# Kernel optimization log

Measured on AMD Instinct MI355X. Metric: run time of the kernel, lower is better.

Reference implementation:

```python
import jax, jax.numpy as jnp
import numpy as np
from jax import lax

BLOCK = 64      # block_size
OVERLAP = 16
NITER = 64      # Niter init kwarg; loop runs min(1000, Niter)
L = 0.24        # diffusion step size
K = 0.03        # exp(logk), logk = log(0.03)
DEPS = 0.1
FFT_STEPS = 10
THRESH = 0.1    # uniform-region variance threshold


def _g(x):
    # g(x) = 1 / (1 + |x^2| / K^2)
    return 1.0 / (1.0 + jnp.abs(x * x) / (K * K))


def _avgpool3(x):
    # F.avg_pool2d(x, 3, stride=1, padding=1) with count_include_pad=True (divide by 9)
    s = lax.reduce_window(x, 0.0, lax.add, (1, 1, 3, 3), (1, 1, 1, 1),
                          [(0, 0), (0, 0), (1, 1), (1, 1)])
    return s / 9.0


def _fft_diffuse_block(block, bcv, bch):
    cv_mean = bcv.mean()
    ch_mean = bch.mean()
    h, w = block.shape[2], block.shape[3]
    ky = jnp.arange(h, dtype=block.dtype)[:, None] * (2.0 * np.pi / h)      # [h,1]
    kx = jnp.arange(w // 2 + 1, dtype=block.dtype)[None, :] * (2.0 * np.pi / w)  # [1,w//2+1]
    op = (1.0 - 2.0 * L * (cv_mean * (1.0 - jnp.cos(ky)) + ch_mean * (1.0 - jnp.cos(kx)))) ** FFT_STEPS
    return jnp.fft.irfft2(jnp.fft.rfft2(block) * op, s=(h, w))


def _forward(guide, initial):
    # depth shift for stability (torch code branches on initial.min() <= deps)
    shift = jnp.where(initial.min() <= DEPS, DEPS, 0.0).astype(initial.dtype)
    depth = initial + shift

    # diffusion coefficients from guide: cv [B,1,H-1,W], ch [B,1,H,W-1]
    cv = _g(jnp.mean(jnp.abs(guide[:, :, 1:, :] - guide[:, :, :-1, :]), axis=1, keepdims=True))
    ch = _g(jnp.mean(jnp.abs(guide[:, :, :, 1:] - guide[:, :, :, :-1]), axis=1, keepdims=True))

    # identify_uniform_regions (local variance via avg pools); original torch code
    # broadcasts shapes (H-1,W) & (H,W-1) which errors -- we crop to common (H-1,W-1)
    cv_var = _avgpool3(cv ** 2) - _avgpool3(cv) ** 2
    ch_var = _avgpool3(ch ** 2) - _avgpool3(ch) ** 2
    uniform = ((cv_var[:, :, :, :-1] < THRESH) & (ch_var[:, :, :-1, :] < THRESH)).astype(depth.dtype)

    B, C, H, W = depth.shape
    step = BLOCK - OVERLAP
    # sequential per-block FFT diffusion with overlap blending (blocks read
    # depth updated by previous blocks, so order matters)
    for b in range(B):
        for y in range(0, H, step):
            for x in range(0, W, step):
                y_end = min(y + BLOCK, H)
                x_end = min(x + BLOCK, W)
                bh, bw = y_end - y, x_end - x
                block = depth[b:b + 1, :, y:y_end, x:x_end]
                bcv = cv[b:b + 1, :, y:y_end - 1, x:x_end]
                bch = ch[b:b + 1, :, y:y_end, x:x_end - 1]
                bun = uniform[b:b + 1, :, y:y_end, x:x_end]  # clips at edges (H-1,W-1)
                cond = bun.mean() > 0.7
                newb = _fft_diffuse_block(block, bcv, bch)
                if y > 0 or x > 0:
                    blend_y = jnp.ones((bh,), depth.dtype)
                    if y > 0:
                        r = jnp.arange(bh)
                        blend_y = jnp.where(r < min(OVERLAP, bh), r.astype(depth.dtype) / OVERLAP, blend_y)
                    blend_x = jnp.ones((bw,), depth.dtype)
                    if x > 0:
                        r = jnp.arange(bw)
                        blend_x = jnp.where(r < min(OVERLAP, bw), r.astype(depth.dtype) / OVERLAP, blend_x)
                    blend = (blend_y[:, None] * blend_x[None, :])[None, None]
                    cand = block * (1.0 - blend) + newb * blend
                else:
                    cand = newb
                region = jnp.where(cond, cand, block)
                depth = depth.at[b:b + 1, :, y:y_end, x:x_end].set(region)

    # explicit anisotropic diffusion stencil, serial data dependence -> lax.scan
    def diffuse_step(I, _):
        dv = I[:, :, 1:, :] - I[:, :, :-1, :]
        dh = I[:, :, :, 1:] - I[:, :, :, :-1]  # computed before vertical update (as in torch)
        tv = L * cv * dv
        I = I.at[:, :, 1:, :].add(-tv).at[:, :, :-1, :].add(tv)
        th = L * ch * dh
        I = I.at[:, :, :, 1:].add(-th).at[:, :, :, :-1].add(th)
        return I, None

    depth, _ = lax.scan(diffuse_step, depth, None, length=min(1000, NITER))
    y_pred = depth - shift
    return y_pred, cv, ch


def setup_inputs() -> dict:
    key = jax.random.key(0)
    k1, k2 = jax.random.split(key)
    guide = jax.random.uniform(k1, (2, 3, 512, 512), dtype=jnp.float32)
    initial = jax.random.uniform(k2, (2, 1, 512, 512), dtype=jnp.float32)
    return {"guide": guide, "initial": initial}


def reference(guide, initial):
    # returns (y_pred, cv, ch) matching {'y_pred':..., 'cv':..., 'ch':...}
    return _forward(guide, initial)
```

## Files before the change

kernel.cpp:

```cpp
#include <hip/hip_runtime.h>
#include <stdint.h>

#define LDIFF 0.24f
#define MAGIC 0x5EED0B0B

constexpr int H = 512, W = 512, NB = 2;
constexpr int HW = H * W;
constexpr int N_D = NB * HW;
constexpr int CVH = 511, CVW = 512;
constexpr int CHH = 512, CHW = 511;
constexpr int N_CV = NB * CVH * CVW;
constexpr int NBLKS = 11;
constexpr int NBT = NB * 121;

__device__ inline float ldc(const float* p) {
    return __hip_atomic_load(p, __ATOMIC_RELAXED, __HIP_MEMORY_SCOPE_AGENT);
}
__device__ inline void stc(float* p, float v) {
    __hip_atomic_store(p, v, __ATOMIC_RELAXED, __HIP_MEMORY_SCOPE_AGENT);
}
__device__ inline int ldci(const int* p) {
    return __hip_atomic_load(p, __ATOMIC_RELAXED, __HIP_MEMORY_SCOPE_AGENT);
}
__device__ inline void stci(int* p, int v) {
    __hip_atomic_store(p, v, __ATOMIC_RELAXED, __HIP_MEMORY_SCOPE_AGENT);
}

__device__ inline float rot_a(float x) {
    return __int_as_float(__builtin_amdgcn_update_dpp(0, __float_as_int(x), 0x134, 0xf, 0xf, false));
}
__device__ inline float rot_b(float x) {
    return __int_as_float(__builtin_amdgcn_update_dpp(0, __float_as_int(x), 0x13c, 0xf, 0xf, false));
}
__device__ inline float sh_a(float x) {
    return __int_as_float(__builtin_amdgcn_update_dpp(0, __float_as_int(x), 0x130, 0xf, 0xf, true));
}
__device__ inline float sh_b(float x) {
    return __int_as_float(__builtin_amdgcn_update_dpp(0, __float_as_int(x), 0x138, 0xf, 0xf, true));
}

#define BSTEP(SRC, DST, LO, HI)                                                   \
    _Pragma("unroll")                                                             \
    for (int m = (LO); m <= (HI); m++) {                                          \
        float hs = rot_a(SRC[m]) + rot_b(SRC[m]);                                 \
        float vs = SRC[m - 1] + SRC[m + 1];                                       \
        DST[m] = fmaf(a, vs, fmaf(bc, hs, c0 * SRC[m]));                          \
    }

#define CSTEP(SRC, DST, LO, HI)                                                   \
    _Pragma("unroll")                                                             \
    for (int m = (LO); m <= (HI); m++) {                                          \
        float Vm = SRC[m] + cve[m] * (SRC[m + 1] - SRC[m])                        \
                          - cve[m - 1] * (SRC[m] - SRC[m - 1]);                   \
        float rA = rot_a(Vm), rB = rot_b(Vm);                                     \
        DST[m] = Vm + Pq[m] * (rB - Vm) - Qq[m] * (Vm - rA);                      \
    }

__global__ __launch_bounds__(256) void kall(
    const float* __restrict__ guide, const float* __restrict__ initial,
    float* __restrict__ cv, float* __restrict__ ch,
    float* __restrict__ D, float* __restrict__ T0, float* __restrict__ T1,
    float* __restrict__ ypred, int* __restrict__ sync_)
{
    __shared__ float cvT[73 * 74];
    __shared__ float chT[73 * 74];
    __shared__ float xT[2][4][5][64];
    __shared__ float xB[2][4][5][64];
    __shared__ float red[12];
    __shared__ float prmS[3];
    __shared__ int ctlS[2];

    const int blk = blockIdx.x;
    const int i = blk / NBLKS, j = blk % NBLKS;
    const int b = blockIdx.y;
    const int tid = threadIdx.x;
    const int lane = tid & 63, wv = tid >> 6;
    const int r0 = wv * 16;
    const int me = b * 121 + blk;

    if (tid == 0) {
        int mg = ldci(&sync_[65536]);
        int pw = ldci(&sync_[65537]);
        ctlS[0] = (mg == MAGIC) ? 1 : 0;
        ctlS[1] = (mg == MAGIC) ? (pw & 1) : 0;
    }
    __syncthreads();
    const int havemg = ctlS[0], par = ctlS[1];
    int* wflag = sync_ + par * 32768;
    int* dflag = wflag + 16384;
    {
        int* oth = sync_ + (par ^ 1) * 32768;
        if (tid < 64) stci(&oth[me * 64 + tid], 0);
        if (tid < 16) stci(&oth[16384 + me * 16 + tid], 0);
        if (!havemg) {
            if (tid < 64) stci(&wflag[me * 64 + tid], 0);
            if (tid < 16) stci(&dflag[me * 16 + tid], 0);
            if (me == 0 && tid == 0) { stci(&sync_[65537], 0); stci(&sync_[65538], 0); }
        }
        asm volatile("s_waitcnt vmcnt(0)" ::: "memory");
    }
    __syncthreads();

    const int y0 = i * 48, x0 = j * 48;
    const int y1 = min(y0 + 64, 512), x1 = min(x0 + 64, 512);
    const int bh = y1 - y0, bw = x1 - x0;
    const int yb = y0 - 8, xb = x0 - 8;
    const float kinv = 1.0f / (0.03f * 0.03f);

    const float* gb = guide + (size_t)b * 3 * HW;
    for (int p = tid; p < 73 * 73; p += 256) {
        int rr = p / 73, cc2 = p - rr * 73;
        int y = yb + rr, x = xb + cc2;
        float cvv = 0.0f, chv = 0.0f;
        if (y >= 0 && y < 512 && x >= 0 && x < 512) {
            const float* g = gb + y * W + x;
            float g0 = g[0], g1 = g[HW], g2 = g[2 * HW];
            if (y < 511) {
                float d = (fabsf(g[W] - g0) + fabsf(g[HW + W] - g1) + fabsf(g[2 * HW + W] - g2)) * (1.0f / 3.0f);
                cvv = 1.0f / (1.0f + d * d * kinv);
            }
            if (x < 511) {
                float d = (fabsf(g[1] - g0) + fabsf(g[HW + 1] - g1) + fabsf(g[2 * HW + 1] - g2)) * (1.0f / 3.0f);
                chv = 1.0f / (1.0f + d * d * kinv);
            }
        }
        cvT[rr * 74 + cc2] = cvv;
        chT[rr * 74 + cc2] = chv;
    }
    __syncthreads();

    {
        int rcv = min(y0 + 48, CVH) - y0, ccv = min(x0 + 48, CVW) - x0;
        float* cvo = cv + b * CVH * CVW;
        for (int p = tid; p < rcv * ccv; p += 256) {
            int r = p / ccv, c = p - r * ccv;
            cvo[(y0 + r) * CVW + x0 + c] = cvT[(r + 8) * 74 + c + 8];
        }
        int rch = min(y0 + 48, CHH) - y0, cch = min(x0 + 48, CHW) - x0;
        float* cho = ch + b * CHH * CHW;
        for (int p = tid; p < rch * cch; p += 256) {
            int r = p / cch, c = p - r * cch;
            cho[(y0 + r) * CHW + x0 + c] = chT[(r + 8) * 74 + c + 8];
        }
    }

    float scv = 0.f, sch = 0.f, sun = 0.f;
    {
        int n = (bh - 1) * bw;
        for (int p = tid; p < n; p += 256) { int r = p / bw, c = p - r * bw; scv += cvT[(r + 8) * 74 + c + 8]; }
    }
    {
        int cols = bw - 1, n = bh * cols;
        for (int p = tid; p < n; p += 256) { int r = p / cols, c = p - r * cols; sch += chT[(r + 8) * 74 + c + 8]; }
    }
    const int ur = min(y1, 511) - y0, uc = min(x1, 511) - x0;
    {
        int n = ur * uc;
        for (int p = tid; p < n; p += 256) {
            int r = p / uc, c = p - r * uc;
            float s1 = 0.f, s2 = 0.f, t1 = 0.f, t2 = 0.f;
            #pragma unroll
            for (int dy = 0; dy < 3; dy++)
                #pragma unroll
                for (int dx = 0; dx < 3; dx++) {
                    float v = cvT[(r + 7 + dy) * 74 + c + 7 + dx]; s1 += v; s2 += v * v;
                    float w2 = chT[(r + 7 + dy) * 74 + c + 7 + dx]; t1 += w2; t2 += w2 * w2;
                }
            float m = s1 * (1.0f / 9.0f);
            float vcv = s2 * (1.0f / 9.0f) - m * m;
            m = t1 * (1.0f / 9.0f);
            float vch = t2 * (1.0f / 9.0f) - m * m;
            if (vcv < 0.1f && vch < 0.1f) sun += 1.f;
        }
    }
    #pragma unroll
    for (int m = 1; m < 64; m <<= 1) {
        scv += __shfl_xor(scv, m);
        sch += __shfl_xor(sch, m);
        sun += __shfl_xor(sun, m);
    }
    if (lane == 0) { red[wv * 3] = scv; red[wv * 3 + 1] = sch; red[wv * 3 + 2] = sun; }
    __syncthreads();
    if (tid == 0) {
        float a0 = red[0] + red[3] + red[6] + red[9];
        float a1 = red[1] + red[4] + red[7] + red[10];
        float a2 = red[2] + red[5] + red[8] + red[11];
        prmS[0] = a0 / (float)((bh - 1) * bw);
        prmS[1] = a1 / (float)(bh * (bw - 1));
        prmS[2] = (a2 / (float)(ur * uc) > 0.7f) ? 1.0f : 0.0f;
    }
    __syncthreads();

    int prb = __builtin_amdgcn_update_dpp(0, lane, 0x134, 0xf, 0xf, false);
    const bool dirL = (prb == ((lane + 63) & 63));

    const bool cond = prmS[2] > 0.5f;
    const float a = LDIFF * prmS[0], bc = LDIFF * prmS[1];
    const float c0 = 1.0f - 2.0f * a - 2.0f * bc;
    float* Db = D + b * HW;
    const float* ini = initial + b * HW;

    const int mh = bh - 1, mw = bw - 1;
    const int ccw = lane & mw;

    if (!cond) {
        #pragma unroll
        for (int k = 0; k < 16; k++) {
            int r = r0 + k;
            if (r < bh && (i == 0 || r >= 16) && lane < bw && (j == 0 || lane >= 16)) {
                int ad = (y0 + r) * W + x0 + lane;
                stc(&Db[ad], ini[ad]);
            }
        }
        asm volatile("s_waitcnt vmcnt(0)" ::: "memory");
        if (lane == 0) {
            stci(&wflag[me * 64 + wv * 16], 1);
            stci(&wflag[me * 64 + wv * 16 + 8], 1);
        }
    } else {
        float u[16], orig[16];
        int addr[16]; bool fD[16];
        #pragma unroll
        for (int k = 0; k < 16; k++) {
            int rr = (r0 + k) & mh;
            addr[k] = (y0 + rr) * W + x0 + ccw;
            fD[k] = (i > 0 && rr < 16) || (j > 0 && ccw < 16);
            if (!fD[k]) orig[k] = ini[addr[k]];
        }
        {
            const int Lw = (r0 & mh) >> 4;
            const bool needU = (i > 0) && ((r0 & mh) < 16);
            bool need = false;
            const int* fp = &wflag[me * 64];
            if (lane == 0) {
                if (j > 0) { need = true; fp = &wflag[(me - 1) * 64 + Lw * 16]; }
            } else if (lane == 1) {
                if (needU) { need = true; fp = &wflag[(me - NBLKS) * 64 + 3 * 16]; }
            } else if (lane == 2) {
                if (needU && j < 10) { need = true; fp = &wflag[(me - NBLKS + 1) * 64 + 3 * 16]; }
            } else if (lane == 3) {
                if (needU && j > 0) { need = true; fp = &wflag[(me - NBLKS - 1) * 64 + 3 * 16]; }
            }
            while (true) {
                int v = need ? ldci(fp) : 1;
                if (__ballot(v == 0) == 0) break;
                __builtin_amdgcn_s_sleep(0);
            }
        }
        #pragma unroll
        for (int k = 0; k < 16; k++) if (fD[k]) orig[k] = ldc(&Db[addr[k]]);
        #pragma unroll
        for (int k = 0; k < 16; k++) u[k] = orig[k];

        float wa[26], wb[26];
        #pragma unroll
        for (int g = 0; g < 2; ++g) {
            #pragma unroll
            for (int q = 0; q < 5; q++) {
                xT[g][wv][q][lane] = u[q];
                xB[g][wv][q][lane] = u[11 + q];
            }
            __syncthreads();
            #pragma unroll
            for (int q = 0; q < 5; q++) {
                wa[q]      = xB[g][(wv + 3) & 3][q][lane];
                wa[21 + q] = xT[g][(wv + 1) & 3][q][lane];
            }
            #pragma unroll
            for (int q = 0; q < 16; q++) wa[5 + q] = u[q];
            BSTEP(wa, wb, 1, 24);
            BSTEP(wb, wa, 2, 23);
            BSTEP(wa, wb, 3, 22);
            BSTEP(wb, wa, 4, 21);
            BSTEP(wa, wb, 5, 20);
            #pragma unroll
            for (int q = 0; q < 16; q++) u[q] = wb[5 + q];
        }

        #pragma unroll
        for (int k = 0; k < 16; k++) {
            int r = r0 + k;
            float byw = (y0 > 0 && r < 16) ? (float)r * (1.0f / 16.0f) : 1.0f;
            float bxw = (x0 > 0 && lane < 16) ? (float)lane * (1.0f / 16.0f) : 1.0f;
            float wgt = byw * bxw;
            u[k] = orig[k] * (1.0f - wgt) + u[k] * wgt;
        }
        #pragma unroll
        for (int k = 0; k < 16; k++) {
            int r = r0 + k;
            bool in = (r < bh && lane < bw);
            bool sc = (bw == 64 && lane >= 48) || (r >= 48);
            if (in && sc) stc(&Db[(y0 + r) * W + x0 + lane], u[k]);
        }
        asm volatile("s_waitcnt vmcnt(0)" ::: "memory");
        if (lane == 0) stci(&wflag[me * 64 + wv * 16], 1);
        #pragma unroll
        for (int k = 0; k < 16; k++) {
            int r = r0 + k;
            bool in = (r < bh && lane < bw);
            bool sc = (bw == 64 && lane >= 48) || (r >= 48);
            if (in && !sc) stc(&Db[(y0 + r) * W + x0 + lane], u[k]);
        }
        asm volatile("s_waitcnt vmcnt(0)" ::: "memory");
        if (lane == 0) stci(&wflag[me * 64 + wv * 16 + 8], 1);
    }
    __syncthreads();

    const int cx = xb + lane;
    const int gxc = min(max(cx, 0), 511);
    int gyA[16];
    #pragma unroll
    for (int k = 0; k < 16; k++) {
        int cy = yb + r0 + k;
        gyA[k] = min(max(cy, 0), 511);
    }
    float cve[24], Pq[24], Qq[24];
    #pragma unroll
    for (int m = 0; m < 24; m++) {
        int rr = r0 + m - 4;
        bool ok = (rr >= 0);
        float cvv = ok ? cvT[rr * 74 + lane] : 0.0f;
        float chh = ok ? chT[rr * 74 + lane] : 0.0f;
        float chl = dirL ? sh_a(chh) : sh_b(chh);
        cve[m] = LDIFF * cvv;
        Pq[m] = LDIFF * (dirL ? chh : chl);
        Qq[m] = LDIFF * (dirL ? chl : chh);
    }

    float* Tb0 = T0 + b * HW;
    float* Tb1 = T1 + b * HW;
    float* ypb = ypred + b * HW;

    const int coreh = min(48, 512 - y0), corew = min(48, 512 - x0);
    const bool laneC = (lane >= 8) && (lane < 8 + corew);
    bool ownc[16], ringk[16];
    #pragma unroll
    for (int k = 0; k < 16; k++) {
        int wr = r0 + k;
        ownc[k] = laneC && (wr >= 8) && (wr < 8 + coreh);
        int cr = wr - 8, cl = lane - 8;
        ringk[k] = ownc[k] && (cr < 8 || cr >= coreh - 8 || cl < 8 || cl >= corew - 8);
    }

    float u[16];
    for (int t = 1; t <= 8; t++) {
        if (wv == 0) {
            bool need = false;
            const int* fp = &wflag[me * 64];
            int thr = 1;
            if (t == 1) {
                if (lane < 36) {
                    int nb = lane >> 2;
                    int di = nb / 3 - 1, dj = nb % 3 - 1;
                    int ni = i + di, nj = j + dj;
                    if ((di | dj) != 0 && ni >= 0 && ni < NBLKS && nj >= 0 && nj < NBLKS) {
                        need = true;
                        fp = &wflag[(b * 121 + ni * NBLKS + nj) * 64 + (lane & 3) * 16 + 8];
                    }
                }
            } else {
                thr = t - 1;
                if (lane < 9) {
                    int di = lane / 3 - 1, dj = lane % 3 - 1;
                    int ni = i + di, nj = j + dj;
                    if ((di | dj) != 0 && ni >= 0 && ni < NBLKS && nj >= 0 && nj < NBLKS) {
                        need = true;
                        fp = &dflag[(b * 121 + ni * NBLKS + nj) * 16];
                    }
                }
            }
            while (true) {
                int v = need ? ldci(fp) : 0x7fffffff;
                if (__ballot(v < thr) == 0) break;
                __builtin_amdgcn_s_sleep(4);
            }
        }
        __syncthreads();
        const float* src = (t == 1) ? Db : (((t - 1) & 1) ? Tb1 : Tb0);
        if (t == 1) {
            #pragma unroll
            for (int k = 0; k < 16; k++) u[k] = ldc(&src[gyA[k] * W + gxc]);
        } else {
            #pragma unroll
            for (int k = 0; k < 16; k++) if (!ownc[k]) u[k] = ldc(&src[gyA[k] * W + gxc]);
        }

        #pragma unroll
        for (int g = 0; g < 2; ++g) {
            #pragma unroll
            for (int q = 0; q < 4; q++) {
                xT[g][wv][q][lane] = u[q];
                xB[g][wv][q][lane] = u[12 + q];
            }
            __syncthreads();
            float wa[24], wb[24];
            #pragma unroll
            for (int q = 0; q < 4; q++) {
                wa[q]      = (wv > 0) ? xB[g][wv - 1][q][lane] : u[0];
                wa[20 + q] = (wv < 3) ? xT[g][wv + 1][q][lane] : u[15];
            }
            #pragma unroll
            for (int q = 0; q < 16; q++) wa[4 + q] = u[q];
            CSTEP(wa, wb, 1, 22);
            CSTEP(wb, wa, 2, 21);
            CSTEP(wa, wb, 3, 20);
            CSTEP(wb, wa, 4, 19);
            #pragma unroll
            for (int q = 0; q < 16; q++) u[q] = wa[4 + q];
        }

        if (t < 8) {
            float* dst = (t & 1) ? Tb1 : Tb0;
            #pragma unroll
            for (int k = 0; k < 16; k++) {
                if (ringk[k]) stc(&dst[(yb + r0 + k) * W + xb + lane], u[k]);
            }
            asm volatile("s_waitcnt vmcnt(0)" ::: "memory");
            __syncthreads();
            if (tid == 0) stci(&dflag[me * 16], t);
        } else {
            #pragma unroll
            for (int k = 0; k < 16; k++) {
                if (ownc[k]) ypb[(yb + r0 + k) * W + xb + lane] = u[k];
            }
        }
    }

    __syncthreads();
    if (tid == 0) {
        int n = __hip_atomic_fetch_add(&sync_[65538], 1, __ATOMIC_RELAXED, __HIP_MEMORY_SCOPE_AGENT);
        if (n == NBT - 1) {
            stci(&sync_[65538], 0);
            stci(&sync_[65537], par ^ 1);
            stci(&sync_[65536], MAGIC);
        }
    }
}

extern "C" void kernel_launch(void* const* d_in, const int* in_sizes, int n_in,
                              void* d_out, int out_size, void* d_ws, size_t ws_size,
                              hipStream_t stream) {
    const float* guide   = (const float*)d_in[0];
    const float* initial = (const float*)d_in[1];
    float* y_pred = (float*)d_out;
    float* cv = y_pred + N_D;
    float* ch = cv + N_CV;

    uint8_t* w = (uint8_t*)d_ws;
    int* sync_ = (int*)w;
    float* D  = (float*)(w + 262656);
    float* T0 = D + N_D;
    float* T1 = T0 + N_D;

    kall<<<dim3(121, NB), 256, 0, stream>>>(guide, initial, cv, ch, D, T0, T1, y_pred, sync_);
}
```

Baseline: 285.4 us.

## Replace per-wave flag handoff with per-element sentinel edge buffers between blocks

Each block now publishes its right and bottom overlap strips into a dedicated edge buffer pre-filled with a -1 sentinel. Neighbours poll the individual values instead of waiting on coarse per-wave completion flags, which lets dependent blocks start as soon as the specific data they need arrives and shortens the serial wavefront across the 11x11 block grid. Non-uniform blocks now go through the same unified path. The change adds clearing of the edge buffer each launch and extra polling loads, and it relies on -1 never being a valid float bit pattern in the data.

After: 525.3 us. 84.1% more time.

```diff
diff --git a/kernel.cpp b/kernel.cpp
--- a/kernel.cpp
+++ b/kernel.cpp
@@ -2,7 +2,7 @@
 #include <stdint.h>
 
 #define LDIFF 0.24f
-#define MAGIC 0x5EED0B0B
+#define MAGIC 0x5EED0C0C
 
 constexpr int H = 512, W = 512, NB = 2;
 constexpr int HW = H * W;
@@ -59,7 +59,8 @@
 __global__ __launch_bounds__(256) void kall(
     const float* __restrict__ guide, const float* __restrict__ initial,
     float* __restrict__ cv, float* __restrict__ ch,
-    float* __restrict__ D, float* __restrict__ T0, float* __restrict__ T1,
+    float* __restrict__ D, float* __restrict__ EDG,
+    float* __restrict__ T0, float* __restrict__ T1,
     float* __restrict__ ypred, int* __restrict__ sync_)
 {
     __shared__ float cvT[73 * 74];
@@ -88,13 +89,20 @@
     const int havemg = ctlS[0], par = ctlS[1];
     int* wflag = sync_ + par * 32768;
     int* dflag = wflag + 16384;
+    float* EDGp = EDG + (size_t)par * NBT * 2048;
     {
         int* oth = sync_ + (par ^ 1) * 32768;
         if (tid < 64) stci(&oth[me * 64 + tid], 0);
         if (tid < 16) stci(&oth[16384 + me * 16 + tid], 0);
+        int* eo = (int*)(EDG + (size_t)(par ^ 1) * NBT * 2048 + (size_t)me * 2048);
+        #pragma unroll
+        for (int q = 0; q < 8; q++) stci(&eo[tid + q * 256], -1);
         if (!havemg) {
             if (tid < 64) stci(&wflag[me * 64 + tid], 0);
             if (tid < 16) stci(&dflag[me * 16 + tid], 0);
+            int* ep = (int*)(EDGp + (size_t)me * 2048);
+            #pragma unroll
+            for (int q = 0; q < 8; q++) stci(&ep[tid + q * 256], -1);
             if (me == 0 && tid == 0) { stci(&sync_[65537], 0); stci(&sync_[65538], 0); }
         }
         asm volatile("s_waitcnt vmcnt(0)" ::: "memory");
@@ -202,56 +210,59 @@
 
     const int mh = bh - 1, mw = bw - 1;
     const int ccw = lane & mw;
-
-    if (!cond) {
-        #pragma unroll
-        for (int k = 0; k < 16; k++) {
-            int r = r0 + k;
-            if (r < bh && (i == 0 || r >= 16) && lane < bw && (j == 0 || lane >= 16)) {
-                int ad = (y0 + r) * W + x0 + lane;
-                stc(&Db[ad], ini[ad]);
-            }
-        }
-        asm volatile("s_waitcnt vmcnt(0)" ::: "memory");
+    const int rr0w = r0 & mh;
+
+    float u[16], orig[16];
+    const bool fD = (i > 0 && rr0w < 16) || (j > 0 && ccw < 16);
+    #pragma unroll
+    for (int k = 0; k < 16; k++) {
+        if (!fD) orig[k] = ini[(y0 + rr0w + k) * W + x0 + ccw];
+    }
+
+    {
+        bool need = false;
+        const int* wp = &sync_[65536];
         if (lane == 0) {
-            stci(&wflag[me * 64 + wv * 16], 1);
-            stci(&wflag[me * 64 + wv * 16 + 8], 1);
-        }
-    } else {
-        float u[16], orig[16];
-        int addr[16]; bool fD[16];
-        #pragma unroll
-        for (int k = 0; k < 16; k++) {
-            int rr = (r0 + k) & mh;
-            addr[k] = (y0 + rr) * W + x0 + ccw;
-            fD[k] = (i > 0 && rr < 16) || (j > 0 && ccw < 16);
-            if (!fD[k]) orig[k] = ini[addr[k]];
-        }
-        {
-            const int Lw = (r0 & mh) >> 4;
-            const bool needU = (i > 0) && ((r0 & mh) < 16);
-            bool need = false;
-            const int* fp = &wflag[me * 64];
-            if (lane == 0) {
-                if (j > 0) { need = true; fp = &wflag[(me - 1) * 64 + Lw * 16]; }
-            } else if (lane == 1) {
-                if (needU) { need = true; fp = &wflag[(me - NBLKS) * 64 + 3 * 16]; }
-            } else if (lane == 2) {
-                if (needU && j < 10) { need = true; fp = &wflag[(me - NBLKS + 1) * 64 + 3 * 16]; }
-            } else if (lane == 3) {
-                if (needU && j > 0) { need = true; fp = &wflag[(me - NBLKS - 1) * 64 + 3 * 16]; }
-            }
-            while (true) {
-                int v = need ? ldci(fp) : 1;
-                if (__ballot(v == 0) == 0) break;
-                __builtin_amdgcn_s_sleep(0);
-            }
-        }
-        #pragma unroll
-        for (int k = 0; k < 16; k++) if (fD[k]) orig[k] = ldc(&Db[addr[k]]);
-        #pragma unroll
-        for (int k = 0; k < 16; k++) u[k] = orig[k];
-
+            if (j > 0) { need = true; wp = (const int*)(EDGp + (size_t)(me - 1) * 2048 + (rr0w + 15) * 16 + 15); }
+        } else if (lane == 1) {
+            if (i > 0 && rr0w < 16) { need = true; wp = (const int*)(EDGp + (size_t)(me - NBLKS) * 2048 + 1024 + 15 * 64 + (bw == 64 ? 47 : bw - 1)); }
+        } else if (lane == 2) {
+            if (i > 0 && rr0w < 16 && j < 10) { need = true; wp = (const int*)(EDGp + (size_t)(me - NBLKS + 1) * 2048 + 1024 + 15 * 64 + 15); }
+        }
+        while (true) {
+            int v = need ? ldci(wp) : 0;
+            if (__ballot(v == -1) == 0) break;
+            __builtin_amdgcn_s_sleep(0);
+        }
+    }
+    {
+        const int* sp0 = nullptr; int strd = 0;
+        if (j > 0 && ccw < 16) {
+            sp0 = (const int*)(EDGp + (size_t)(me - 1) * 2048 + rr0w * 16 + ccw);
+            strd = 16;
+        } else if (i > 0 && rr0w < 16) {
+            sp0 = (ccw >= 48) ? (const int*)(EDGp + (size_t)(me - NBLKS + 1) * 2048 + 1024 + (ccw - 48))
+                              : (const int*)(EDGp + (size_t)(me - NBLKS) * 2048 + 1024 + ccw);
+            strd = 64;
+        }
+        uint32_t pend = sp0 ? 0xFFFFu : 0u;
+        while (pend) {
+            int sv[16];
+            #pragma unroll
+            for (int k = 0; k < 16; k++) if (pend & (1u << k)) sv[k] = ldci(sp0 + k * strd);
+            uint32_t np = 0;
+            #pragma unroll
+            for (int k = 0; k < 16; k++) if (pend & (1u << k)) {
+                if (sv[k] != -1) orig[k] = __int_as_float(sv[k]); else np |= 1u << k;
+            }
+            pend = np;
+            if (pend) __builtin_amdgcn_s_sleep(1);
+        }
+    }
+    #pragma unroll
+    for (int k = 0; k < 16; k++) u[k] = orig[k];
+
+    if (cond) {
         float wa[26], wb[26];
         #pragma unroll
         for (int g = 0; g < 2; ++g) {
@@ -276,7 +287,6 @@
             #pragma unroll
             for (int q = 0; q < 16; q++) u[q] = wb[5 + q];
         }
-
         #pragma unroll
         for (int k = 0; k < 16; k++) {
             int r = r0 + k;
@@ -285,25 +295,50 @@
             float wgt = byw * bxw;
             u[k] = orig[k] * (1.0f - wgt) + u[k] * wgt;
         }
+    }
+
+    {
+        float* RGm = EDGp + (size_t)me * 2048;
+        float* BGm = RGm + 1024;
         #pragma unroll
         for (int k = 0; k < 16; k++) {
             int r = r0 + k;
-            bool in = (r < bh && lane < bw);
-            bool sc = (bw == 64 && lane >= 48) || (r >= 48);
-            if (in && sc) stc(&Db[(y0 + r) * W + x0 + lane], u[k]);
-        }
-        asm volatile("s_waitcnt vmcnt(0)" ::: "memory");
-        if (lane == 0) stci(&wflag[me * 64 + wv * 16], 1);
+            if (r < bh && lane < bw) {
+                if (bw == 64 && lane >= 48) stc(&RGm[r * 16 + (lane - 48)], u[k]);
+                if (r >= 48)                stc(&BGm[(r - 48) * 64 + lane], u[k]);
+            }
+        }
+    }
+    #pragma unroll
+    for (int k = 0; k < 16; k++) {
+        int r = r0 + k;
+        if (r < bh && lane < bw && (i == 0 || r >= 16) && (j == 0 || lane >= 16))
+            stc(&Db[(y0 + r) * W + x0 + lane], u[k]);
+    }
+    if (r0 < bh) {
+        bool need = false;
+        const int* fp = &sync_[65536];
+        if (lane == 0) {
+            if (j > 0) { need = true; fp = &wflag[(me - 1) * 64 + wv * 16 + 8]; }
+        } else if (lane == 1) {
+            if (wv == 0 && i > 0) { need = true; fp = &wflag[(me - NBLKS) * 64 + 3 * 16 + 8]; }
+        } else if (lane == 2) {
+            if (wv == 0 && i > 0 && j < 10) { need = true; fp = &wflag[(me - NBLKS + 1) * 64 + 3 * 16 + 8]; }
+        }
+        while (true) {
+            int v = need ? ldci(fp) : 1;
+            if (__ballot(v == 0) == 0) break;
+            __builtin_amdgcn_s_sleep(0);
+        }
         #pragma unroll
         for (int k = 0; k < 16; k++) {
             int r = r0 + k;
-            bool in = (r < bh && lane < bw);
-            bool sc = (bw == 64 && lane >= 48) || (r >= 48);
-            if (in && !sc) stc(&Db[(y0 + r) * W + x0 + lane], u[k]);
-        }
-        asm volatile("s_waitcnt vmcnt(0)" ::: "memory");
-        if (lane == 0) stci(&wflag[me * 64 + wv * 16 + 8], 1);
-    }
+            if (r < bh && lane < bw && !((i == 0 || r >= 16) && (j == 0 || lane >= 16)))
+                stc(&Db[(y0 + r) * W + x0 + lane], u[k]);
+        }
+    }
+    asm volatile("s_waitcnt vmcnt(0)" ::: "memory");
+    if (lane == 0) stci(&wflag[me * 64 + wv * 16 + 8], 1);
     __syncthreads();
 
     const int cx = xb + lane;
@@ -342,7 +377,7 @@
         ringk[k] = ownc[k] && (cr < 8 || cr >= coreh - 8 || cl < 8 || cl >= corew - 8);
     }
 
-    float u[16];
+    float uq[16];
     for (int t = 1; t <= 8; t++) {
         if (wv == 0) {
             bool need = false;
@@ -379,41 +414,41 @@
         const float* src = (t == 1) ? Db : (((t - 1) & 1) ? Tb1 : Tb0);
         if (t == 1) {
             #pragma unroll
-            for (int k = 0; k < 16; k++) u[k] = ldc(&src[gyA[k] * W + gxc]);
+            for (int k = 0; k < 16; k++) uq[k] = ldc(&src[gyA[k] * W + gxc]);
         } else {
             #pragma unroll
-            for (int k = 0; k < 16; k++) if (!ownc[k]) u[k] = ldc(&src[gyA[k] * W + gxc]);
+            for (int k = 0; k < 16; k++) if (!ownc[k]) uq[k] = ldc(&src[gyA[k] * W + gxc]);
         }
 
         #pragma unroll
         for (int g = 0; g < 2; ++g) {
             #pragma unroll
             for (int q = 0; q < 4; q++) {
-                xT[g][wv][q][lane] = u[q];
-                xB[g][wv][q][lane] = u[12 + q];
+                xT[g][wv][q][lane] = uq[q];
+                xB[g][wv][q][lane] = uq[12 + q];
             }
             __syncthreads();
             float wa[24], wb[24];
             #pragma unroll
             for (int q = 0; q < 4; q++) {
-                wa[q]      = (wv > 0) ? xB[g][wv - 1][q][lane] : u[0];
-                wa[20 + q] = (wv < 3) ? xT[g][wv + 1][q][lane] : u[15];
-            }
-            #pragma unroll
-            for (int q = 0; q < 16; q++) wa[4 + q] = u[q];
+                wa[q]      = (wv > 0) ? xB[g][wv - 1][q][lane] : uq[0];
+                wa[20 + q] = (wv < 3) ? xT[g][wv + 1][q][lane] : uq[15];
+            }
+            #pragma unroll
+            for (int q = 0; q < 16; q++) wa[4 + q] = uq[q];
             CSTEP(wa, wb, 1, 22);
             CSTEP(wb, wa, 2, 21);
             CSTEP(wa, wb, 3, 20);
             CSTEP(wb, wa, 4, 19);
             #pragma unroll
-            for (int q = 0; q < 16; q++) u[q] = wa[4 + q];
+            for (int q = 0; q < 16; q++) uq[q] = wa[4 + q];
         }
 
         if (t < 8) {
             float* dst = (t & 1) ? Tb1 : Tb0;
             #pragma unroll
             for (int k = 0; k < 16; k++) {
-                if (ringk[k]) stc(&dst[(yb + r0 + k) * W + xb + lane], u[k]);
+                if (ringk[k]) stc(&dst[(yb + r0 + k) * W + xb + lane], uq[k]);
             }
             asm volatile("s_waitcnt vmcnt(0)" ::: "memory");
             __syncthreads();
@@ -421,7 +456,7 @@
         } else {
             #pragma unroll
             for (int k = 0; k < 16; k++) {
-                if (ownc[k]) ypb[(yb + r0 + k) * W + xb + lane] = u[k];
+                if (ownc[k]) ypb[(yb + r0 + k) * W + xb + lane] = uq[k];
             }
         }
     }
@@ -448,9 +483,10 @@
 
     uint8_t* w = (uint8_t*)d_ws;
     int* sync_ = (int*)w;
-    float* D  = (float*)(w + 262656);
-    float* T0 = D + N_D;
-    float* T1 = T0 + N_D;
-
-    kall<<<dim3(121, NB), 256, 0, stream>>>(guide, initial, cv, ch, D, T0, T1, y_pred, sync_);
-}
+    float* EDG = (float*)(w + 262656);
+    float* D   = EDG + (size_t)2 * NBT * 2048;
+    float* T0  = D + N_D;
+    float* T1  = T0 + N_D;
+
+    kall<<<dim3(121, NB), 256, 0, stream>>>(guide, initial, cv, ch, D, EDG, T0, T1, y_pred, sync_);
+}
```
